# Kernel optimization log

Measured on AMD Instinct MI355X. Metric: run time of the kernel, lower is better.

Reference implementation:

```python
import jax, jax.numpy as jnp
import numpy as np

N = 131072   # batch
D = 32       # num features (main subnets)
P = 32       # num interaction pairs
H_MAIN = 64  # hidden_dim_main
H_INTER = 64 # hidden_dim_inter


def setup_inputs() -> dict:
    key = jax.random.key(0)
    ks = jax.random.split(key, 7)
    X = jax.random.normal(ks[0], (N, D), dtype=jnp.float32)
    # cyclic interaction pairs (i, (i+1) % D), matching init_kwargs literal
    pairs = jnp.asarray(np.stack([np.arange(P), (np.arange(P) + 1) % D], axis=1), dtype=jnp.int32)
    # stacked ExU params for the D main subnets: log_weight [H,1] -> [D,H], bias [1] -> [D]
    log_w_main = (jax.random.normal(ks[1], (D, H_MAIN), dtype=jnp.float32) * 0.1)
    bias_main = jnp.zeros((D,), dtype=jnp.float32)
    v_main = jax.random.normal(ks[2], (D, H_MAIN), dtype=jnp.float32) / np.float32(np.sqrt(H_MAIN))
    # stacked ExU params for the P interaction subnets: log_weight [H,2], bias [2]
    log_w_inter = (jax.random.normal(ks[3], (P, H_INTER, 2), dtype=jnp.float32) * 0.1)
    bias_inter = jnp.zeros((P, 2), dtype=jnp.float32)
    v_inter = jax.random.normal(ks[4], (P, H_INTER), dtype=jnp.float32) / np.float32(np.sqrt(H_INTER))
    # final Linear(D+P, 1)
    W_final = jax.random.normal(ks[5], (D + P,), dtype=jnp.float32) / np.float32(np.sqrt(D + P))
    b_final = jnp.zeros((), dtype=jnp.float32)
    return {
        "X": X,
        "log_w_main": log_w_main,
        "bias_main": bias_main,
        "v_main": v_main,
        "log_w_inter": log_w_inter,
        "bias_inter": bias_inter,
        "v_inter": v_inter,
        "W_final": W_final,
        "b_final": b_final,
        "pairs": pairs,
    }


def reference(X, log_w_main, bias_main, v_main, log_w_inter, bias_inter, v_inter, W_final, b_final, pairs):
    # Main subnets, batched over features: ExU(1,H) is (x - b) * exp(log_w)
    h_main = jax.nn.silu((X - bias_main[None, :])[:, :, None] * jnp.exp(log_w_main)[None, :, :])  # [N,D,H]
    m_out = jnp.einsum('ndh,dh->nd', h_main, v_main)  # [N,D]
    # Interaction subnets, batched over pairs: gather the 2 columns per pair
    Xp = X[:, pairs]  # [N,P,2]
    h_int = jax.nn.silu(jnp.einsum('npc,phc->nph', Xp - bias_inter[None, :, :], jnp.exp(log_w_inter)))  # [N,P,H]
    i_out = jnp.einsum('nph,ph->np', h_int, v_inter)  # [N,P]
    Z = jnp.concatenate([m_out, i_out], axis=1)  # [N, D+P]
    out = Z @ W_final + b_final  # [N]
    return out, Z
```

## Files before the change

### kernel.cpp

```cpp
#include <hip/hip_runtime.h>

#define DD 32
#define PP 32
#define HH 64
#define TPB 512
#define ROWS 512

#define M_NE 128
#define M_LO (-8.0f)
#define M_HI (8.0f)
#define I_NE 96
#define I_LO (-6.5f)
#define I_HI (6.5f)
#define I_CELLS (I_NE * I_NE)

#define BTPB 256
#define MAIN_BLOCKS ((DD * M_NE) / BTPB)
#define BLOCKS_PER_P (I_CELLS / BTPB)
#define INTER_BLOCKS (PP * BLOCKS_PER_P)

#define TSTR 36
#define XSTR 33

__device__ __forceinline__ float silu_fast(float t) {
    const float LOG2E = 1.4426950408889634f;
    return t * __builtin_amdgcn_rcpf(1.f + __builtin_amdgcn_exp2f(-t * LOG2E));
}

__device__ __forceinline__ unsigned short f2bf(float f) {
    unsigned u = __float_as_uint(f);
    u += 0x7FFF + ((u >> 16) & 1);
    return (unsigned short)(u >> 16);
}

__device__ __forceinline__ float bf2f(unsigned short s) {
    return __uint_as_float((unsigned)s << 16);
}

__global__ void build_luts(const float* __restrict__ lwm,
                           const float* __restrict__ vm,
                           const float* __restrict__ lwi,
                           const float* __restrict__ vi,
                           float* __restrict__ LUTm,
                           unsigned short* __restrict__ LUTi)
{
    const float LOG2E = 1.4426950408889634f;
    __shared__ float2 sew[HH];
    __shared__ float  sv[HH];

    if (blockIdx.x < MAIN_BLOCKS) {
        const float h = (M_HI - M_LO) / (float)(M_NE - 1);
        int idx = blockIdx.x * BTPB + threadIdx.x;
        int d = idx >> 7;
        int i = idx & (M_NE - 1);
        float s = M_LO + (float)i * h;
        float acc = 0.f;
        #pragma unroll 8
        for (int k = 0; k < HH; ++k) {
            float w = __builtin_amdgcn_exp2f(lwm[d * HH + k] * LOG2E);
            acc = fmaf(silu_fast(s * w), vm[d * HH + k], acc);
        }
        LUTm[idx] = acc;
    } else {
        const float h = (I_HI - I_LO) / (float)(I_NE - 1);
        const int rel = blockIdx.x - MAIN_BLOCKS;
        const int p   = rel / BLOCKS_PER_P;
        const int cip = (rel % BLOCKS_PER_P) * BTPB + threadIdx.x;
        const int i   = cip / I_NE;
        const int j   = cip - i * I_NE;
        if (threadIdx.x < HH) {
            int t = threadIdx.x;
            sew[t] = make_float2(
                __builtin_amdgcn_exp2f(lwi[(p * HH + t) * 2 + 0] * LOG2E),
                __builtin_amdgcn_exp2f(lwi[(p * HH + t) * 2 + 1] * LOG2E));
            sv[t] = vi[p * HH + t];
        }
        __syncthreads();
        float c0 = I_LO + (float)i * h;
        float c1 = I_LO + (float)j * h;
        float acc = 0.f;
        #pragma unroll 8
        for (int k = 0; k < HH; ++k) {
            float a = fmaf(c0, sew[k].x, c1 * sew[k].y);
            acc = fmaf(silu_fast(a), sv[k], acc);
        }
        unsigned short ab = f2bf(acc);
        unsigned short* cb = LUTi + (size_t)p * I_CELLS * 4;
        if (i < I_NE - 1 && j < I_NE - 1) cb[((i    ) * I_NE + j    ) * 4 + 0] = ab;
        if (i < I_NE - 1 && j > 0)        cb[((i    ) * I_NE + j - 1) * 4 + 1] = ab;
        if (i > 0        && j < I_NE - 1) cb[((i - 1) * I_NE + j    ) * 4 + 2] = ab;
        if (i > 0        && j > 0)        cb[((i - 1) * I_NE + j - 1) * 4 + 3] = ab;
    }
}

#define IEVAL(PIDX, ZVAR) do {                                               \
    const int p_  = (PIDX);                                                  \
    const int i0_ = s_p0[p_], i1_ = s_p1[p_];                                \
    float u_  = fmaf(s_x[r][i0_], I_INVH, s_io0[p_]);                        \
    float w_  = fmaf(s_x[r][i1_], I_INVH, s_io1[p_]);                        \
    int iu_ = (int)floorf(u_);                                               \
    int iv_ = (int)floorf(w_);                                               \
    iu_ = iu_ < 0 ? 0 : (iu_ > I_NE - 2 ? I_NE - 2 : iu_);                   \
    iv_ = iv_ < 0 ? 0 : (iv_ > I_NE - 2 ? I_NE - 2 : iv_);                   \
    float fu_ = u_ - (float)iu_;                                             \
    float fv_ = w_ - (float)iv_;                                             \
    ushort4 cell_ = LUTi[(size_t)p_ * I_CELLS + iu_ * I_NE + iv_];           \
    float a00_ = bf2f(cell_.x), a01_ = bf2f(cell_.y);                        \
    float a10_ = bf2f(cell_.z), a11_ = bf2f(cell_.w);                        \
    float r0_ = fmaf(fv_, a01_ - a00_, a00_);                                \
    float r1_ = fmaf(fv_, a11_ - a10_, a10_);                                \
    ZVAR = fmaf(fu_, r1_ - r0_, r0_);                                        \
    dot = fmaf(ZVAR, s_wf[DD + p_], dot);                                    \
} while (0)

__global__ __launch_bounds__(TPB, 2) void qgam_main(
    const float* __restrict__ X,
    const float* __restrict__ bias_main,
    const float* __restrict__ bias_inter,
    const float* __restrict__ W_final,
    const float* __restrict__ b_final,
    const int* __restrict__ pairs,
    const float* __restrict__ LUTm,
    const ushort4* __restrict__ LUTi,
    float* __restrict__ out,
    float* __restrict__ Zout,
    int nrows)
{
    const float M_INVH = (float)(M_NE - 1) / (M_HI - M_LO);
    const float I_INVH = (float)(I_NE - 1) / (I_HI - I_LO);

    __shared__ float s_lutm[DD * M_NE];
    __shared__ float s_x[ROWS][XSTR];
    __shared__ float s_t[ROWS][TSTR];
    __shared__ float s_wf[DD + PP];
    __shared__ float s_moff[DD];
    __shared__ float s_io0[PP], s_io1[PP];
    __shared__ int   s_p0[PP], s_p1[PP];

    const int tid  = threadIdx.x;
    const int base = blockIdx.x * ROWS;

    {
        const float4* __restrict__ lm4 = reinterpret_cast<const float4*>(LUTm);
        float4* __restrict__ sl4 = reinterpret_cast<float4*>(s_lutm);
        #pragma unroll
        for (int k = 0; k < 2; ++k)
            sl4[k * TPB + tid] = lm4[k * TPB + tid];
    }
    {
        const float4* __restrict__ Xv =
            reinterpret_cast<const float4*>(X) + (size_t)base * (DD / 4);
        #pragma unroll
        for (int k = 0; k < 8; ++k) {
            const int fi = k * TPB + tid;
            const int rl = fi >> 3;
            const int c  = (fi & 7) * 4;
            if (base + rl < nrows) {
                float4 v = Xv[fi];
                s_x[rl][c + 0] = v.x;
                s_x[rl][c + 1] = v.y;
                s_x[rl][c + 2] = v.z;
                s_x[rl][c + 3] = v.w;
            }
        }
    }
    if (tid < DD + PP) s_wf[tid] = W_final[tid];
    if (tid < PP) {
        s_moff[tid] = -(bias_main[tid] + M_LO) * M_INVH;
        s_io0[tid]  = -(bias_inter[2 * tid + 0] + I_LO) * I_INVH;
        s_io1[tid]  = -(bias_inter[2 * tid + 1] + I_LO) * I_INVH;
        s_p0[tid]   = pairs[2 * tid + 0];
        s_p1[tid]   = pairs[2 * tid + 1];
    }
    __syncthreads();

    const int r = tid;
    const int n = base + r;

    float dot = b_final[0];

    #pragma unroll
    for (int d4 = 0; d4 < DD / 4; ++d4) {
        float z[4];
        #pragma unroll
        for (int j = 0; j < 4; ++j) {
            const int d = d4 * 4 + j;
            float u  = fmaf(s_x[r][d], M_INVH, s_moff[d]);
            int   ii = (int)floorf(u);
            ii = ii < 0 ? 0 : (ii > M_NE - 2 ? M_NE - 2 : ii);
            float f  = u - (float)ii;
            float t0 = s_lutm[(d << 7) + ii];
            float t1 = s_lutm[(d << 7) + ii + 1];
            z[j] = fmaf(f, t1 - t0, t0);
            dot = fmaf(z[j], s_wf[d], dot);
        }
        *reinterpret_cast<float4*>(&s_t[r][d4 * 4]) =
            make_float4(z[0], z[1], z[2], z[3]);
    }

    __syncthreads();
    #pragma unroll
    for (int i = 0; i < 8; ++i) {
        const int fi   = i * TPB + tid;
        const int rowl = fi >> 3;
        const int c4   = (fi & 7) * 4;
        const int row  = base + rowl;
        if (row < nrows) {
            float4 v = *reinterpret_cast<const float4*>(&s_t[rowl][c4]);
            *reinterpret_cast<float4*>(&Zout[(size_t)row * (DD + PP) + c4]) = v;
        }
    }
    __syncthreads();

    #pragma unroll 1
    for (int p4 = 0; p4 < PP / 4; ++p4) {
        const int pb = p4 * 4;
        float z0, z1, z2, z3;
        IEVAL(pb + 0, z0); __syncthreads();
        IEVAL(pb + 1, z1); __syncthreads();
        IEVAL(pb + 2, z2); __syncthreads();
        IEVAL(pb + 3, z3); __syncthreads();
        *reinterpret_cast<float4*>(&s_t[r][pb]) = make_float4(z0, z1, z2, z3);
    }

    if (n < nrows) out[n] = dot;

    __syncthreads();
    #pragma unroll
    for (int i = 0; i < 8; ++i) {
        const int fi   = i * TPB + tid;
        const int rowl = fi >> 3;
        const int c4   = (fi & 7) * 4;
        const int row  = base + rowl;
        if (row < nrows) {
            float4 v = *reinterpret_cast<const float4*>(&s_t[rowl][c4]);
            *reinterpret_cast<float4*>(&Zout[(size_t)row * (DD + PP) + DD + c4]) = v;
        }
    }
}

extern "C" void kernel_launch(void* const* d_in, const int* in_sizes, int n_in,
                              void* d_out, int out_size, void* d_ws, size_t ws_size,
                              hipStream_t stream) {
    const float* X   = (const float*)d_in[0];
    const float* lwm = (const float*)d_in[1];
    const float* bm  = (const float*)d_in[2];
    const float* vm  = (const float*)d_in[3];
    const float* lwi = (const float*)d_in[4];
    const float* bi  = (const float*)d_in[5];
    const float* vi  = (const float*)d_in[6];
    const float* wf  = (const float*)d_in[7];
    const float* bf  = (const float*)d_in[8];
    const int* pairs = (const int*)d_in[9];

    const int nrows = in_sizes[0] / DD;
    float* out = (float*)d_out;
    float* Z   = out + nrows;

    float*          LUTm = (float*)d_ws;
    unsigned short* LUTi = (unsigned short*)((char*)d_ws +
                           ((DD * M_NE * sizeof(float) + 255) & ~255));

    build_luts<<<MAIN_BLOCKS + INTER_BLOCKS, BTPB, 0, stream>>>(lwm, vm, lwi, vi,
                                                                LUTm, LUTi);

    const int grid = (nrows + ROWS - 1) / ROWS;
    qgam_main<<<grid, TPB, 0, stream>>>(X, bm, bi, wf, bf, pairs, LUTm,
                                        (const ushort4*)LUTi, out, Z, nrows);
}
```

Before: 32.72 us.

## Fuse LUT build and evaluation into one cooperative persistent kernel

Replaces the separate LUT-building kernel and the main kernel with a single cooperative kernel. Blocks first build the LUT slices in a grid-stride loop, then do a grid-wide sync, then walk row tiles persistently with a grid capped at 256 blocks. This removes one kernel launch and the inter-kernel gap. In exchange it adds the cost of a grid barrier, requires cooperative-launch residency, and gives each block several tiles, which reduces parallel slack.

```diff
diff --git a/kernel.cpp b/kernel.cpp
--- a/kernel.cpp
+++ b/kernel.cpp
@@ -1,4 +1,7 @@
 #include <hip/hip_runtime.h>
+#include <hip/hip_cooperative_groups.h>
+
+namespace cg = cooperative_groups;
 
 #define DD 32
 #define PP 32
@@ -14,10 +17,9 @@
 #define I_HI (6.5f)
 #define I_CELLS (I_NE * I_NE)
 
-#define BTPB 256
-#define MAIN_BLOCKS ((DD * M_NE) / BTPB)
-#define BLOCKS_PER_P (I_CELLS / BTPB)
-#define INTER_BLOCKS (PP * BLOCKS_PER_P)
+#define VB_MAIN ((DD * M_NE) / TPB)
+#define VB_PER_P (I_CELLS / TPB)
+#define VB_TOTAL (VB_MAIN + PP * VB_PER_P)
 
 #define TSTR 36
 #define XSTR 33
@@ -35,62 +37,6 @@
 
 __device__ __forceinline__ float bf2f(unsigned short s) {
     return __uint_as_float((unsigned)s << 16);
-}
-
-__global__ void build_luts(const float* __restrict__ lwm,
-                           const float* __restrict__ vm,
-                           const float* __restrict__ lwi,
-                           const float* __restrict__ vi,
-                           float* __restrict__ LUTm,
-                           unsigned short* __restrict__ LUTi)
-{
-    const float LOG2E = 1.4426950408889634f;
-    __shared__ float2 sew[HH];
-    __shared__ float  sv[HH];
-
-    if (blockIdx.x < MAIN_BLOCKS) {
-        const float h = (M_HI - M_LO) / (float)(M_NE - 1);
-        int idx = blockIdx.x * BTPB + threadIdx.x;
-        int d = idx >> 7;
-        int i = idx & (M_NE - 1);
-        float s = M_LO + (float)i * h;
-        float acc = 0.f;
-        #pragma unroll 8
-        for (int k = 0; k < HH; ++k) {
-            float w = __builtin_amdgcn_exp2f(lwm[d * HH + k] * LOG2E);
-            acc = fmaf(silu_fast(s * w), vm[d * HH + k], acc);
-        }
-        LUTm[idx] = acc;
-    } else {
-        const float h = (I_HI - I_LO) / (float)(I_NE - 1);
-        const int rel = blockIdx.x - MAIN_BLOCKS;
-        const int p   = rel / BLOCKS_PER_P;
-        const int cip = (rel % BLOCKS_PER_P) * BTPB + threadIdx.x;
-        const int i   = cip / I_NE;
-        const int j   = cip - i * I_NE;
-        if (threadIdx.x < HH) {
-            int t = threadIdx.x;
-            sew[t] = make_float2(
-                __builtin_amdgcn_exp2f(lwi[(p * HH + t) * 2 + 0] * LOG2E),
-                __builtin_amdgcn_exp2f(lwi[(p * HH + t) * 2 + 1] * LOG2E));
-            sv[t] = vi[p * HH + t];
-        }
-        __syncthreads();
-        float c0 = I_LO + (float)i * h;
-        float c1 = I_LO + (float)j * h;
-        float acc = 0.f;
-        #pragma unroll 8
-        for (int k = 0; k < HH; ++k) {
-            float a = fmaf(c0, sew[k].x, c1 * sew[k].y);
-            acc = fmaf(silu_fast(a), sv[k], acc);
-        }
-        unsigned short ab = f2bf(acc);
-        unsigned short* cb = LUTi + (size_t)p * I_CELLS * 4;
-        if (i < I_NE - 1 && j < I_NE - 1) cb[((i    ) * I_NE + j    ) * 4 + 0] = ab;
-        if (i < I_NE - 1 && j > 0)        cb[((i    ) * I_NE + j - 1) * 4 + 1] = ab;
-        if (i > 0        && j < I_NE - 1) cb[((i - 1) * I_NE + j    ) * 4 + 2] = ab;
-        if (i > 0        && j > 0)        cb[((i - 1) * I_NE + j - 1) * 4 + 3] = ab;
-    }
 }
 
 #define IEVAL(PIDX, ZVAR) do {                                               \
@@ -104,7 +50,7 @@
     iv_ = iv_ < 0 ? 0 : (iv_ > I_NE - 2 ? I_NE - 2 : iv_);                   \
     float fu_ = u_ - (float)iu_;                                             \
     float fv_ = w_ - (float)iv_;                                             \
-    ushort4 cell_ = LUTi[(size_t)p_ * I_CELLS + iu_ * I_NE + iv_];           \
+    ushort4 cell_ = LUTi4[(size_t)p_ * I_CELLS + iu_ * I_NE + iv_];          \
     float a00_ = bf2f(cell_.x), a01_ = bf2f(cell_.y);                        \
     float a10_ = bf2f(cell_.z), a11_ = bf2f(cell_.w);                        \
     float r0_ = fmaf(fv_, a01_ - a00_, a00_);                                \
@@ -113,19 +59,24 @@
     dot = fmaf(ZVAR, s_wf[DD + p_], dot);                                    \
 } while (0)
 
-__global__ __launch_bounds__(TPB, 2) void qgam_main(
+__global__ __launch_bounds__(TPB, 2) void qgam_fused(
     const float* __restrict__ X,
+    const float* __restrict__ lwm,
     const float* __restrict__ bias_main,
+    const float* __restrict__ vm,
+    const float* __restrict__ lwi,
     const float* __restrict__ bias_inter,
+    const float* __restrict__ vi,
     const float* __restrict__ W_final,
     const float* __restrict__ b_final,
     const int* __restrict__ pairs,
-    const float* __restrict__ LUTm,
-    const ushort4* __restrict__ LUTi,
+    float* __restrict__ LUTm,
+    unsigned short* __restrict__ LUTi,
     float* __restrict__ out,
     float* __restrict__ Zout,
     int nrows)
 {
+    const float LOG2E  = 1.4426950408889634f;
     const float M_INVH = (float)(M_NE - 1) / (M_HI - M_LO);
     const float I_INVH = (float)(I_NE - 1) / (I_HI - I_LO);
 
@@ -137,8 +88,61 @@
     __shared__ float s_io0[PP], s_io1[PP];
     __shared__ int   s_p0[PP], s_p1[PP];
 
-    const int tid  = threadIdx.x;
-    const int base = blockIdx.x * ROWS;
+    const int tid = threadIdx.x;
+
+    {
+        float2* sew = reinterpret_cast<float2*>(&s_t[0][0]);
+        float*  sv  = reinterpret_cast<float*>(&s_t[0][0]) + 128;
+
+        for (int vb = blockIdx.x; vb < VB_TOTAL; vb += gridDim.x) {
+            if (vb < VB_MAIN) {
+                const float h = (M_HI - M_LO) / (float)(M_NE - 1);
+                int idx = vb * TPB + tid;
+                int d = idx >> 7;
+                int i = idx & (M_NE - 1);
+                float s = M_LO + (float)i * h;
+                float acc = 0.f;
+                #pragma unroll 8
+                for (int k = 0; k < HH; ++k) {
+                    float w = __builtin_amdgcn_exp2f(lwm[d * HH + k] * LOG2E);
+                    acc = fmaf(silu_fast(s * w), vm[d * HH + k], acc);
+                }
+                LUTm[idx] = acc;
+            } else {
+                const float h = (I_HI - I_LO) / (float)(I_NE - 1);
+                const int rel = vb - VB_MAIN;
+                const int p   = rel / VB_PER_P;
+                const int cip = (rel % VB_PER_P) * TPB + tid;
+                const int i   = cip / I_NE;
+                const int j   = cip - i * I_NE;
+                if (tid < HH) {
+                    sew[tid] = make_float2(
+                        __builtin_amdgcn_exp2f(lwi[(p * HH + tid) * 2 + 0] * LOG2E),
+                        __builtin_amdgcn_exp2f(lwi[(p * HH + tid) * 2 + 1] * LOG2E));
+                    sv[tid] = vi[p * HH + tid];
+                }
+                __syncthreads();
+                float c0 = I_LO + (float)i * h;
+                float c1 = I_LO + (float)j * h;
+                float acc = 0.f;
+                #pragma unroll 8
+                for (int k = 0; k < HH; ++k) {
+                    float a = fmaf(c0, sew[k].x, c1 * sew[k].y);
+                    acc = fmaf(silu_fast(a), sv[k], acc);
+                }
+                unsigned short ab = f2bf(acc);
+                unsigned short* cb = LUTi + (size_t)p * I_CELLS * 4;
+                if (i < I_NE - 1 && j < I_NE - 1) cb[((i    ) * I_NE + j    ) * 4 + 0] = ab;
+                if (i < I_NE - 1 && j > 0)        cb[((i    ) * I_NE + j - 1) * 4 + 1] = ab;
+                if (i > 0        && j < I_NE - 1) cb[((i - 1) * I_NE + j    ) * 4 + 2] = ab;
+                if (i > 0        && j > 0)        cb[((i - 1) * I_NE + j - 1) * 4 + 3] = ab;
+                __syncthreads();
+            }
+        }
+    }
+
+    __threadfence();
+    cg::this_grid().sync();
 
     {
         const float4* __restrict__ lm4 = reinterpret_cast<const float4*>(LUTm);
@@ -146,23 +150,6 @@
         #pragma unroll
         for (int k = 0; k < 2; ++k)
             sl4[k * TPB + tid] = lm4[k * TPB + tid];
-    }
-    {
-        const float4* __restrict__ Xv =
-            reinterpret_cast<const float4*>(X) + (size_t)base * (DD / 4);
-        #pragma unroll
-        for (int k = 0; k < 8; ++k) {
-            const int fi = k * TPB + tid;
-            const int rl = fi >> 3;
-            const int c  = (fi & 7) * 4;
-            if (base + rl < nrows) {
-                float4 v = Xv[fi];
-                s_x[rl][c + 0] = v.x;
-                s_x[rl][c + 1] = v.y;
-                s_x[rl][c + 2] = v.z;
-                s_x[rl][c + 3] = v.w;
-            }
-        }
     }
     if (tid < DD + PP) s_wf[tid] = W_final[tid];
     if (tid < PP) {
@@ -172,69 +159,91 @@
         s_p0[tid]   = pairs[2 * tid + 0];
         s_p1[tid]   = pairs[2 * tid + 1];
     }
-    __syncthreads();
-
-    const int r = tid;
-    const int n = base + r;
-
-    float dot = b_final[0];
-
-    #pragma unroll
-    for (int d4 = 0; d4 < DD / 4; ++d4) {
-        float z[4];
-        #pragma unroll
-        for (int j = 0; j < 4; ++j) {
-            const int d = d4 * 4 + j;
-            float u  = fmaf(s_x[r][d], M_INVH, s_moff[d]);
-            int   ii = (int)floorf(u);
-            ii = ii < 0 ? 0 : (ii > M_NE - 2 ? M_NE - 2 : ii);
-            float f  = u - (float)ii;
-            float t0 = s_lutm[(d << 7) + ii];
-            float t1 = s_lutm[(d << 7) + ii + 1];
-            z[j] = fmaf(f, t1 - t0, t0);
-            dot = fmaf(z[j], s_wf[d], dot);
-        }
-        *reinterpret_cast<float4*>(&s_t[r][d4 * 4]) =
-            make_float4(z[0], z[1], z[2], z[3]);
-    }
-
-    __syncthreads();
-    #pragma unroll
-    for (int i = 0; i < 8; ++i) {
-        const int fi   = i * TPB + tid;
-        const int rowl = fi >> 3;
-        const int c4   = (fi & 7) * 4;
-        const int row  = base + rowl;
-        if (row < nrows) {
-            float4 v = *reinterpret_cast<const float4*>(&s_t[rowl][c4]);
-            *reinterpret_cast<float4*>(&Zout[(size_t)row * (DD + PP) + c4]) = v;
-        }
-    }
-    __syncthreads();
-
-    #pragma unroll 1
-    for (int p4 = 0; p4 < PP / 4; ++p4) {
-        const int pb = p4 * 4;
-        float z0, z1, z2, z3;
-        IEVAL(pb + 0, z0); __syncthreads();
-        IEVAL(pb + 1, z1); __syncthreads();
-        IEVAL(pb + 2, z2); __syncthreads();
-        IEVAL(pb + 3, z3); __syncthreads();
-        *reinterpret_cast<float4*>(&s_t[r][pb]) = make_float4(z0, z1, z2, z3);
-    }
-
-    if (n < nrows) out[n] = dot;
-
-    __syncthreads();
-    #pragma unroll
-    for (int i = 0; i < 8; ++i) {
-        const int fi   = i * TPB + tid;
-        const int rowl = fi >> 3;
-        const int c4   = (fi & 7) * 4;
-        const int row  = base + rowl;
-        if (row < nrows) {
-            float4 v = *reinterpret_cast<const float4*>(&s_t[rowl][c4]);
-            *reinterpret_cast<float4*>(&Zout[(size_t)row * (DD + PP) + DD + c4]) = v;
+    const ushort4* __restrict__ LUTi4 = reinterpret_cast<const ushort4*>(LUTi);
+
+    for (int base = blockIdx.x * ROWS; base < nrows; base += gridDim.x * ROWS) {
+        __syncthreads();
+
+        {
+            const float4* __restrict__ Xv =
+                reinterpret_cast<const float4*>(X) + (size_t)base * (DD / 4);
+            #pragma unroll
+            for (int k = 0; k < 8; ++k) {
+                const int fi = k * TPB + tid;
+                const int rl = fi >> 3;
+                const int c  = (fi & 7) * 4;
+                if (base + rl < nrows) {
+                    float4 v = Xv[fi];
+                    s_x[rl][c + 0] = v.x;
+                    s_x[rl][c + 1] = v.y;
+                    s_x[rl][c + 2] = v.z;
+                    s_x[rl][c + 3] = v.w;
+                }
+            }
+        }
+        __syncthreads();
+
+        const int r = tid;
+        const int n = base + r;
+        float dot = b_final[0];
+
+        #pragma unroll
+        for (int d4 = 0; d4 < DD / 4; ++d4) {
+            float z[4];
+            #pragma unroll
+            for (int j = 0; j < 4; ++j) {
+                const int d = d4 * 4 + j;
+                float u  = fmaf(s_x[r][d], M_INVH, s_moff[d]);
+                int   ii = (int)floorf(u);
+                ii = ii < 0 ? 0 : (ii > M_NE - 2 ? M_NE - 2 : ii);
+                float f  = u - (float)ii;
+                float t0 = s_lutm[(d << 7) + ii];
+                float t1 = s_lutm[(d << 7) + ii + 1];
+                z[j] = fmaf(f, t1 - t0, t0);
+                dot = fmaf(z[j], s_wf[d], dot);
+            }
+            *reinterpret_cast<float4*>(&s_t[r][d4 * 4]) =
+                make_float4(z[0], z[1], z[2], z[3]);
+        }
+
+        __syncthreads();
+        #pragma unroll
+        for (int i = 0; i < 8; ++i) {
+            const int fi   = i * TPB + tid;
+            const int rowl = fi >> 3;
+            const int c4   = (fi & 7) * 4;
+            const int row  = base + rowl;
+            if (row < nrows) {
+                float4 v = *reinterpret_cast<const float4*>(&s_t[rowl][c4]);
+                *reinterpret_cast<float4*>(&Zout[(size_t)row * (DD + PP) + c4]) = v;
+            }
+        }
+        __syncthreads();
+
+        #pragma unroll 1
+        for (int p4 = 0; p4 < PP / 4; ++p4) {
+            const int pb = p4 * 4;
+            float z0, z1, z2, z3;
+            IEVAL(pb + 0, z0); __syncthreads();
+            IEVAL(pb + 1, z1); __syncthreads();
+            IEVAL(pb + 2, z2); __syncthreads();
+            IEVAL(pb + 3, z3); __syncthreads();
+            *reinterpret_cast<float4*>(&s_t[r][pb]) = make_float4(z0, z1, z2, z3);
+        }
+
+        if (n < nrows) out[n] = dot;
+
+        __syncthreads();
+        #pragma unroll
+        for (int i = 0; i < 8; ++i) {
+            const int fi   = i * TPB + tid;
+            const int rowl = fi >> 3;
+            const int c4   = (fi & 7) * 4;
+            const int row  = base + rowl;
+            if (row < nrows) {
+                float4 v = *reinterpret_cast<const float4*>(&s_t[rowl][c4]);
+                *reinterpret_cast<float4*>(&Zout[(size_t)row * (DD + PP) + DD + c4]) = v;
+            }
         }
     }
 }
@@ -253,7 +262,7 @@
     const float* bf  = (const float*)d_in[8];
     const int* pairs = (const int*)d_in[9];
 
-    const int nrows = in_sizes[0] / DD;
+    int nrows = in_sizes[0] / DD;
     float* out = (float*)d_out;
     float* Z   = out + nrows;
 
@@ -261,10 +270,14 @@
     unsigned short* LUTi = (unsigned short*)((char*)d_ws +
                            ((DD * M_NE * sizeof(float) + 255) & ~255));
 
-    build_luts<<<MAIN_BLOCKS + INTER_BLOCKS, BTPB, 0, stream>>>(lwm, vm, lwi, vi,
-                                                                LUTm, LUTi);
-
-    const int grid = (nrows + ROWS - 1) / ROWS;
-    qgam_main<<<grid, TPB, 0, stream>>>(X, bm, bi, wf, bf, pairs, LUTm,
-                                        (const ushort4*)LUTi, out, Z, nrows);
-}
+    int ntiles = (nrows + ROWS - 1) / ROWS;
+    int grid   = ntiles < 256 ? ntiles : 256;
+
+    void* args[] = {
+        (void*)&X, (void*)&lwm, (void*)&bm, (void*)&vm, (void*)&lwi,
+        (void*)&bi, (void*)&vi, (void*)&wf, (void*)&bf, (void*)&pairs,
+        (void*)&LUTm, (void*)&LUTi, (void*)&out, (void*)&Z, (void*)&nrows
+    };
+    hipLaunchCooperativeKernel((const void*)qgam_fused, dim3(grid), dim3(TPB),
+                               args, 0, stream);
+}
```

After: 125.6 us. +283.7%, slower.
